# Kernel tuning notes

Hardware: AMD Instinct MI355X
Metric: run time of the kernel (lower is better)

Reference implementation:

```python
import jax, jax.numpy as jnp
import numpy as np

B, P, D, A = 256, 196, 512, 512

def setup_inputs() -> dict:
    key = jax.random.key(0)
    ks = jax.random.split(key, 12)
    sc = 1.0 / np.sqrt(D)
    sa = 1.0 / np.sqrt(A)
    return {
        "encoder_out": jax.random.normal(ks[0], (B, P, D), jnp.float32),
        "decoder_hidden": jax.random.normal(ks[1], (B, D), jnp.float32),
        "st": jax.random.normal(ks[2], (B, D), jnp.float32),
        "Wv": jax.random.normal(ks[3], (D, A), jnp.float32) * sc,
        "bv": jnp.zeros((A,), jnp.float32),
        "Wh": jax.random.normal(ks[4], (D, A), jnp.float32) * sc,
        "bh": jnp.zeros((A,), jnp.float32),
        "Ws": jax.random.normal(ks[5], (D, A), jnp.float32) * sc,
        "bs": jnp.zeros((A,), jnp.float32),
        "Wav": jax.random.normal(ks[6], (A,), jnp.float32) * sa,
        "bav": jnp.zeros((), jnp.float32),
        "Was": jax.random.normal(ks[7], (A,), jnp.float32) * sa,
        "bas": jnp.zeros((), jnp.float32),
    }

def reference(encoder_out, decoder_hidden, st, Wv, bv, Wh, bh, Ws, bs, Wav, bav, Was, bas):
    # hidden: (B, A)
    hidden = decoder_hidden @ Wh + bh
    # v: (B, P, A)
    v = jnp.einsum('bpd,da->bpa', encoder_out, Wv) + bv
    # z_t: (B, P) -- additive attention scores over pixels
    z_t = jnp.einsum('bpa,a->bp', jnp.tanh(v + hidden[:, None, :]), Wav) + bav
    alpha_t = jax.nn.softmax(z_t, axis=1)
    # c_t: (B, D) -- attention-weighted encoding
    c_t = jnp.einsum('bpd,bp->bd', encoder_out, alpha_t)
    # sentinel branch: s (B, A), s_att (B, 1)
    s = st @ Ws + bs
    s_att = jnp.tanh(s + hidden) @ Was + bas  # (B,)
    z_t_extended = jnp.concatenate([z_t, s_att[:, None]], axis=1)  # (B, P+1)
    alpha_t_hat = jax.nn.softmax(z_t_extended, axis=1)
    beta_t = alpha_t_hat[:, -1:]  # (B, 1)
    c_hat_t = beta_t * st + (1.0 - beta_t) * c_t
    return (c_hat_t, alpha_t, beta_t)
```

## Files before the change

kernel.cpp:

```cpp
#include <hip/hip_runtime.h>
#include <hip/hip_bf16.h>
#include <cstdint>

#define B_ 256
#define P_ 196
#define D_ 512
#define A_ 512

#define OUT_CHAT  0
#define OUT_ALPHA (B_*D_)
#define OUT_BETA  (B_*D_ + B_*P_)

typedef unsigned short ushort_t;
typedef uint32_t u32;
typedef uint64_t u64;
typedef __attribute__((ext_vector_type(8))) __bf16 bf16x8;
typedef __attribute__((ext_vector_type(4))) float f32x4;

__device__ __forceinline__ ushort_t f2bf(float f) {
    union { float f; u32 i; } v; v.f = f;
    u32 r = (v.i + 0x7fffu + ((v.i >> 16) & 1u)) >> 16;
    return (ushort_t)r;
}
__device__ __forceinline__ float bfbits2f(u32 lo16) {
    union { u32 i; float f; } v; v.i = lo16 << 16; return v.f;
}
__device__ __forceinline__ u32 cvt2bf(float x, float y) {
    union { __hip_bfloat162 h; u32 u; } v;
    v.h = __float22bfloat162_rn(make_float2(x, y));
    return v.u;
}
__device__ __forceinline__ float tanh_fast(float x) {
    float e = __expf(2.0f * x);
    return 1.0f - 2.0f / (e + 1.0f);
}
__device__ __forceinline__ void async_load16(const ushort_t* g, ushort_t* l) {
    __builtin_amdgcn_global_load_lds(
        (const __attribute__((address_space(1))) unsigned int*)g,
        (__attribute__((address_space(3))) unsigned int*)l, 16, 0, 0);
}
__device__ __forceinline__ void fma8(float ap, uint4 v, float ac[8]) {
    ac[0] = fmaf(ap, bfbits2f(v.x & 0xffffu), ac[0]);
    ac[1] = fmaf(ap, bfbits2f(v.x >> 16),     ac[1]);
    ac[2] = fmaf(ap, bfbits2f(v.y & 0xffffu), ac[2]);
    ac[3] = fmaf(ap, bfbits2f(v.y >> 16),     ac[3]);
    ac[4] = fmaf(ap, bfbits2f(v.z & 0xffffu), ac[4]);
    ac[5] = fmaf(ap, bfbits2f(v.z >> 16),     ac[5]);
    ac[6] = fmaf(ap, bfbits2f(v.w & 0xffffu), ac[6]);
    ac[7] = fmaf(ap, bfbits2f(v.w >> 16),     ac[7]);
}

__global__ __launch_bounds__(256) void k_prep(
    const float* __restrict__ E, const float* __restrict__ dh,
    const float* __restrict__ st,
    const float* __restrict__ Wv, const float* __restrict__ Wh,
    const float* __restrict__ Ws,
    ushort_t* __restrict__ Ebf, ushort_t* __restrict__ dhbf,
    ushort_t* __restrict__ stbf,
    ushort_t* __restrict__ WvT, ushort_t* __restrict__ WhT,
    ushort_t* __restrict__ WsT)
{
    __shared__ ushort_t tile[32][33];
    int bx = blockIdx.x;
    if (bx < 12544) {
        size_t i0 = (size_t)bx * 512 + threadIdx.x;
        const float4* src = (const float4*)E;
        u64* dst = (u64*)Ebf;
        float4 v0 = src[i0];
        float4 v1 = src[i0 + 256];
        dst[i0]       = (u64)cvt2bf(v0.x, v0.y) | ((u64)cvt2bf(v0.z, v0.w) << 32);
        dst[i0 + 256] = (u64)cvt2bf(v1.x, v1.y) | ((u64)cvt2bf(v1.z, v1.w) << 32);
    } else if (bx < 12672) {
        int gid = (bx - 12544) * 256 + threadIdx.x;
        float4 dv = ((const float4*)dh)[gid];
        float4 sv = ((const float4*)st)[gid];
        ((u64*)dhbf)[gid] = (u64)cvt2bf(dv.x, dv.y) | ((u64)cvt2bf(dv.z, dv.w) << 32);
        ((u64*)stbf)[gid] = (u64)cvt2bf(sv.x, sv.y) | ((u64)cvt2bf(sv.z, sv.w) << 32);
    } else {
        int idx = bx - 12672;
        int z   = idx >> 8;
        int rem = idx & 255;
        int tby = rem >> 4, tbx = rem & 15;
        const float* W  = (z == 0) ? Wv  : (z == 1) ? Wh  : Ws;
        ushort_t*    WT = (z == 0) ? WvT : (z == 1) ? WhT : WsT;
        int t = threadIdx.x, r = t >> 5, c = t & 31;
#pragma unroll
        for (int i = 0; i < 4; ++i) {
            int row = r + 8 * i;
            tile[row][c] = f2bf(W[(size_t)(tby * 32 + row) * A_ + tbx * 32 + c]);
        }
        __syncthreads();
#pragma unroll
        for (int i = 0; i < 4; ++i) {
            int row = r + 8 * i;
            WT[(size_t)(tbx * 32 + row) * D_ + tby * 32 + c] = tile[c][row];
        }
    }
}

#define PADK 72

__global__ __launch_bounds__(256) void k1_mfma(
    const ushort_t* __restrict__ dhbf, const ushort_t* __restrict__ stbf,
    const ushort_t* __restrict__ WhT,  const ushort_t* __restrict__ WsT,
    const float* __restrict__ bh, const float* __restrict__ bs,
    float* __restrict__ hidden_ws, float* __restrict__ s_ws)
{
    __shared__ ushort_t As[128 * PADK];
    __shared__ ushort_t Bs[128 * PADK];

    int mat = blockIdx.z;
    const ushort_t* Abf = mat ? stbf : dhbf;
    const ushort_t* WT  = mat ? WsT  : WhT;
    const float*    bia = mat ? bs   : bh;
    float*          outp = mat ? s_ws : hidden_ws;

    int tid = threadIdx.x;
    int m0 = blockIdx.y * 128;
    int n0 = blockIdx.x * 128;

    int lane = tid & 63, w = tid >> 6;
    int wm = w & 1, wn = w >> 1;
    int col = lane & 15, q = lane >> 4;

    f32x4 acc[4][4];
#pragma unroll
    for (int tm = 0; tm < 4; ++tm)
#pragma unroll
        for (int tn = 0; tn < 4; ++tn)
            acc[tm][tn] = (f32x4){0.f, 0.f, 0.f, 0.f};

    const ushort_t* arow = As + (wm * 64 + col) * PADK + q * 8;
    const ushort_t* brow = Bs + (wn * 64 + col) * PADK + q * 8;

    int sr = tid >> 3, sc = tid & 7;
    for (int kt = 0; kt < D_ / 64; ++kt) {
#pragma unroll
        for (int i = 0; i < 4; ++i) {
            int row = sr + i * 32;
            *(uint4*)(As + row * PADK + sc * 8) =
                *(const uint4*)(Abf + (size_t)(m0 + row) * D_ + kt * 64 + sc * 8);
            *(uint4*)(Bs + row * PADK + sc * 8) =
                *(const uint4*)(WT + (size_t)(n0 + row) * D_ + kt * 64 + sc * 8);
        }
        __syncthreads();
#pragma unroll
        for (int ks = 0; ks < 2; ++ks) {
            bf16x8 afr[4];
#pragma unroll
            for (int tm = 0; tm < 4; ++tm)
                afr[tm] = *(const bf16x8*)(arow + tm * 16 * PADK + ks * 32);
#pragma unroll
            for (int tn = 0; tn < 4; ++tn) {
                bf16x8 bfr = *(const bf16x8*)(brow + tn * 16 * PADK + ks * 32);
#pragma unroll
                for (int tm = 0; tm < 4; ++tm)
                    acc[tm][tn] = __builtin_amdgcn_mfma_f32_16x16x32_bf16(
                        afr[tm], bfr, acc[tm][tn], 0, 0, 0);
            }
        }
        __syncthreads();
    }

#pragma unroll
    for (int tm = 0; tm < 4; ++tm)
#pragma unroll
        for (int r = 0; r < 4; ++r) {
            int b = m0 + wm * 64 + tm * 16 + q * 4 + r;
#pragma unroll
            for (int tn = 0; tn < 4; ++tn) {
                int n = n0 + wn * 64 + tn * 16 + col;
                outp[(size_t)b * A_ + n] = acc[tm][tn][r] + bia[n];
            }
        }
}

#define BM3 64
__global__ __launch_bounds__(256, 2) void k2_z_bf(
    const ushort_t* __restrict__ Ebf, const ushort_t* __restrict__ WvT,
    const float* __restrict__ hidden_ws, const float* __restrict__ bv,
    const float* __restrict__ Wav, float* __restrict__ z_ws)
{
    __shared__ ushort_t As[BM3 * 512];
    __shared__ float hv_s[2][A_];
    __shared__ float wav_s[A_];
    __shared__ float zpart[4][BM3];

    int tid = threadIdx.x;
    int m0 = blockIdx.x * BM3;
    int b0 = m0 / P_, b1 = (m0 + BM3 - 1) / P_;

#pragma unroll
    for (int j = 0; j < 2; ++j) {
        int a = j * 256 + tid;
        float bva = bv[a];
        hv_s[0][a] = hidden_ws[(size_t)b0 * A_ + a] + bva;
        hv_s[1][a] = hidden_ws[(size_t)b1 * A_ + a] + bva;
        wav_s[a]   = Wav[a];
    }

    int lane = tid & 63, w = tid >> 6;
    int col = lane & 15, q = lane >> 4;

    {
        int r0 = tid >> 6, sc = tid & 63;
#pragma unroll
        for (int i = 0; i < 16; ++i) {
            int row  = i * 4 + r0;
            int slot = sc ^ (row & 7);
            async_load16(Ebf + (size_t)(m0 + row) * D_ + slot * 8,
                         As + i * 2048 + tid * 8);
        }
    }
    asm volatile("s_waitcnt vmcnt(0)" ::: "memory");
    __builtin_amdgcn_s_barrier();

    f32x4 acc[4][8];
#pragma unroll
    for (int tm = 0; tm < 4; ++tm)
#pragma unroll
        for (int tn = 0; tn < 8; ++tn)
            acc[tm][tn] = (f32x4){0.f, 0.f, 0.f, 0.f};

    int fx = col & 7;
    const ushort_t* bgp = WvT + (size_t)(w * 128 + col) * D_ + q * 8;

#pragma unroll
    for (int k32 = 0; k32 < 16; ++k32) {
        bf16x8 afr[4];
#pragma unroll
        for (int tm = 0; tm < 4; ++tm)
            afr[tm] = *(const bf16x8*)(As + (tm * 16 + col) * 512
                                          + (((k32 * 4 + q) ^ fx) * 8));
#pragma unroll
        for (int tn = 0; tn < 8; ++tn) {
            bf16x8 bfr = *(const bf16x8*)(bgp + (size_t)tn * 16 * D_ + k32 * 32);
#pragma unroll
            for (int tm = 0; tm < 4; ++tm)
                acc[tm][tn] = __builtin_amdgcn_mfma_f32_16x16x32_bf16(
                    afr[tm], bfr, acc[tm][tn], 0, 0, 0);
        }
    }

#pragma unroll
    for (int tm = 0; tm < 4; ++tm) {
#pragma unroll
        for (int r = 0; r < 4; ++r) {
            int row = tm * 16 + q * 4 + r;
            int bsel = ((m0 + row) / P_) - b0;
            float zr = 0.f;
#pragma unroll
            for (int tn = 0; tn < 8; ++tn) {
                int nl = w * 128 + tn * 16 + col;
                zr += wav_s[nl] * tanh_fast(acc[tm][tn][r] + hv_s[bsel][nl]);
            }
#pragma unroll
            for (int msk = 1; msk < 16; msk <<= 1)
                zr += __shfl_xor(zr, msk, 64);
            if (col == 0) zpart[w][row] = zr;
        }
    }
    __syncthreads();
    if (tid < BM3)
        z_ws[m0 + tid] = zpart[0][tid] + zpart[1][tid]
                       + zpart[2][tid] + zpart[3][tid];
}

__global__ __launch_bounds__(512) void k34_softmax_ct(
    const ushort_t* __restrict__ Ebf, const float* __restrict__ st,
    const float* __restrict__ z_ws, const float* __restrict__ hidden_ws,
    const float* __restrict__ s_ws, const float* __restrict__ Was,
    const float* __restrict__ bas, const float* __restrict__ bav,
    float* __restrict__ out)
{
    __shared__ float red[8];
    __shared__ float al[P_];
    __shared__ float acc_s[8][516];
    __shared__ float bm_s, bl_s, sa_s;

    int b = blockIdx.x, t = threadIdx.x;
    int lane = t & 63, w = t >> 6;

    float part = Was[t] * tanh_fast(s_ws[(size_t)b * A_ + t]
                                  + hidden_ws[(size_t)b * A_ + t]);
#pragma unroll
    for (int o = 32; o >= 1; o >>= 1) part += __shfl_down(part, o, 64);
    if (lane == 0) red[w] = part;
    __syncthreads();
    if (t == 0) {
        float s = 0.f;
#pragma unroll
        for (int i = 0; i < 8; ++i) s += red[i];
        sa_s = s + bas[0];
    }
    __syncthreads();

    float zv = (t < P_) ? (z_ws[(size_t)b * P_ + t] + bav[0]) : -1e30f;
    float m = zv;
#pragma unroll
    for (int o = 32; o >= 1; o >>= 1) m = fmaxf(m, __shfl_xor(m, o, 64));
    if (lane == 0) red[w] = m;
    __syncthreads();
    if (t == 0) {
        float mm = red[0];
#pragma unroll
        for (int i = 1; i < 8; ++i) mm = fmaxf(mm, red[i]);
        bm_s = mm;
    }
    __syncthreads();
    float m1 = bm_s;
    float e = (t < P_) ? __expf(zv - m1) : 0.f;
    float s = e;
#pragma unroll
    for (int o = 32; o >= 1; o >>= 1) s += __shfl_xor(s, o, 64);
    if (lane == 0) red[w] = s;
    __syncthreads();
    if (t == 0) {
        float ss = 0.f;
#pragma unroll
        for (int i = 0; i < 8; ++i) ss += red[i];
        bl_s = ss;
    }
    __syncthreads();
    float l1 = bl_s;
    if (t < P_) {
        float alpha = e / l1;
        al[t] = alpha;
        out[OUT_ALPHA + (size_t)b * P_ + t] = alpha;
    }
    float sa = sa_s;
    float m2 = fmaxf(m1, sa);
    float eb2 = __expf(sa - m2);
    float l2 = __expf(m1 - m2) * l1 + eb2;
    float beta = eb2 / l2;
    if (t == 0) out[OUT_BETA + b] = beta;
    __syncthreads();

    float ac[8] = {0.f, 0.f, 0.f, 0.f, 0.f, 0.f, 0.f, 0.f};
    const uint4* eb = (const uint4*)(Ebf + (size_t)b * P_ * D_);
#pragma unroll 4
    for (int i = 0; i < 24; ++i) {
        int pp = w + 8 * i;
        uint4 v = eb[(size_t)pp * (D_ / 8) + lane];
        fma8(al[pp], v, ac);
    }
    if (w < P_ - 192) {
        int pp = 192 + w;
        uint4 v = eb[(size_t)pp * (D_ / 8) + lane];
        fma8(al[pp], v, ac);
    }
#pragma unroll
    for (int j = 0; j < 8; ++j) acc_s[w][lane * 8 + j] = ac[j];
    __syncthreads();
    float c = 0.f;
#pragma unroll
    for (int g = 0; g < 8; ++g) c += acc_s[g][t];
    float sv = st[(size_t)b * D_ + t];
    out[OUT_CHAT + (size_t)b * D_ + t] = beta * sv + (1.f - beta) * c;
}

extern "C" void kernel_launch(void* const* d_in, const int* in_sizes, int n_in,
                              void* d_out, int out_size, void* d_ws, size_t ws_size,
                              hipStream_t stream)
{
    (void)in_sizes; (void)n_in; (void)out_size; (void)ws_size;
    const float* E   = (const float*)d_in[0];
    const float* dh  = (const float*)d_in[1];
    const float* st  = (const float*)d_in[2];
    const float* Wv  = (const float*)d_in[3];
    const float* bv  = (const float*)d_in[4];
    const float* Wh  = (const float*)d_in[5];
    const float* bh  = (const float*)d_in[6];
    const float* Ws  = (const float*)d_in[7];
    const float* bs  = (const float*)d_in[8];
    const float* Wav = (const float*)d_in[9];
    const float* bav = (const float*)d_in[10];
    const float* Was = (const float*)d_in[11];
    const float* bas = (const float*)d_in[12];
    float* out = (float*)d_out;

    char* ws = (char*)d_ws;
    ushort_t* WvT     = (ushort_t*)(ws);
    ushort_t* WhT     = (ushort_t*)(ws + 524288);
    ushort_t* WsT     = (ushort_t*)(ws + 1048576);
    float*    z_w     = (float*)(ws + 524288);
    ushort_t* dhbf    = (ushort_t*)(ws + 1572864);
    ushort_t* stbf    = (ushort_t*)(ws + 1835008);
    float*    hidden_w= (float*)(ws + 2097152);
    float*    s_w     = (float*)(ws + 2621440);
    ushort_t* Ebf     = (ushort_t*)(ws + 3145728);

    k_prep<<<12544 + 128 + 768, 256, 0, stream>>>(E, dh, st, Wv, Wh, Ws,
                                                  Ebf, dhbf, stbf, WvT, WhT, WsT);
    k1_mfma<<<dim3(4, 2, 2), 256, 0, stream>>>(dhbf, stbf, WhT, WsT, bh, bs,
                                               hidden_w, s_w);
    k2_z_bf<<<(B_ * P_) / BM3, 256, 0, stream>>>(
        Ebf, WvT, hidden_w, bv, Wav, z_w);
    k34_softmax_ct<<<256, 512, 0, stream>>>(Ebf, st, z_w, hidden_w, s_w,
                                            Was, bas, bav, out);
}
```

Baseline: 289.3 us.

## Split k2 score GEMM across 8 waves with 2x4 warp tiling

Doubles the k2_z_bf block to 512 threads and splits the 64-row tile across two wave rows, so each wave computes 32 rows by 128 columns instead of 64 by 128. The LDS A tile is reorganised into eight K-slices of 64 columns each, with an XOR swizzle, to match the new per-thread load pattern. This halves per-wave accumulator registers and adds waves to hide latency, but each WvT B fragment is now loaded by two waves, doubling global B traffic per block.

```diff
diff --git a/kernel.cpp b/kernel.cpp
--- a/kernel.cpp
+++ b/kernel.cpp
@@ -176,12 +176,12 @@
 }
 
 #define BM3 64
-__global__ __launch_bounds__(256, 2) void k2_z_bf(
+__global__ __launch_bounds__(512) void k2_z_bf(
     const ushort_t* __restrict__ Ebf, const ushort_t* __restrict__ WvT,
     const float* __restrict__ hidden_ws, const float* __restrict__ bv,
     const float* __restrict__ Wav, float* __restrict__ z_ws)
 {
-    __shared__ ushort_t As[BM3 * 512];
+    __shared__ ushort_t As[8][BM3 * 64];
     __shared__ float hv_s[2][A_];
     __shared__ float wav_s[A_];
     __shared__ float zpart[4][BM3];
@@ -190,9 +190,8 @@
     int m0 = blockIdx.x * BM3;
     int b0 = m0 / P_, b1 = (m0 + BM3 - 1) / P_;
 
-#pragma unroll
-    for (int j = 0; j < 2; ++j) {
-        int a = j * 256 + tid;
+    {
+        int a = tid;
         float bva = bv[a];
         hv_s[0][a] = hidden_ws[(size_t)b0 * A_ + a] + bva;
         hv_s[1][a] = hidden_ws[(size_t)b1 * A_ + a] + bva;
@@ -200,64 +199,64 @@
     }
 
     int lane = tid & 63, w = tid >> 6;
+    int wm = w & 1, wn = w >> 1;
     int col = lane & 15, q = lane >> 4;
 
     {
-        int r0 = tid >> 6, sc = tid & 63;
-#pragma unroll
-        for (int i = 0; i < 16; ++i) {
-            int row  = i * 4 + r0;
-            int slot = sc ^ (row & 7);
-            async_load16(Ebf + (size_t)(m0 + row) * D_ + slot * 8,
-                         As + i * 2048 + tid * 8);
-        }
+        int sr = tid >> 3, spos = tid & 7;
+        int gch = spos ^ (sr & 7);
+        const ushort_t* agb = Ebf + (size_t)(m0 + sr) * D_ + gch * 8;
+#pragma unroll
+        for (int kt = 0; kt < 8; ++kt)
+            async_load16(agb + kt * 64, &As[kt][0] + tid * 8);
     }
     asm volatile("s_waitcnt vmcnt(0)" ::: "memory");
     __builtin_amdgcn_s_barrier();
 
-    f32x4 acc[4][8];
-#pragma unroll
-    for (int tm = 0; tm < 4; ++tm)
+    f32x4 acc[2][8];
+#pragma unroll
+    for (int tm = 0; tm < 2; ++tm)
 #pragma unroll
         for (int tn = 0; tn < 8; ++tn)
             acc[tm][tn] = (f32x4){0.f, 0.f, 0.f, 0.f};
 
     int fx = col & 7;
-    const ushort_t* bgp = WvT + (size_t)(w * 128 + col) * D_ + q * 8;
+    const ushort_t* bgp = WvT + (size_t)(wn * 128 + col) * D_ + q * 8;
 
 #pragma unroll
     for (int k32 = 0; k32 < 16; ++k32) {
-        bf16x8 afr[4];
-#pragma unroll
-        for (int tm = 0; tm < 4; ++tm)
-            afr[tm] = *(const bf16x8*)(As + (tm * 16 + col) * 512
-                                          + (((k32 * 4 + q) ^ fx) * 8));
+        int kt = k32 >> 1, ks = k32 & 1;
+        bf16x8 afr[2];
+#pragma unroll
+        for (int tm = 0; tm < 2; ++tm)
+            afr[tm] = *(const bf16x8*)(&As[kt][0]
+                + (wm * 32 + tm * 16 + col) * 64 + (((ks * 4 + q) ^ fx) * 8));
 #pragma unroll
         for (int tn = 0; tn < 8; ++tn) {
             bf16x8 bfr = *(const bf16x8*)(bgp + (size_t)tn * 16 * D_ + k32 * 32);
 #pragma unroll
-            for (int tm = 0; tm < 4; ++tm)
+            for (int tm = 0; tm < 2; ++tm)
                 acc[tm][tn] = __builtin_amdgcn_mfma_f32_16x16x32_bf16(
                     afr[tm], bfr, acc[tm][tn], 0, 0, 0);
         }
     }
 
 #pragma unroll
-    for (int tm = 0; tm < 4; ++tm) {
+    for (int tm = 0; tm < 2; ++tm) {
 #pragma unroll
         for (int r = 0; r < 4; ++r) {
-            int row = tm * 16 + q * 4 + r;
+            int row = wm * 32 + tm * 16 + q * 4 + r;
             int bsel = ((m0 + row) / P_) - b0;
             float zr = 0.f;
 #pragma unroll
             for (int tn = 0; tn < 8; ++tn) {
-                int nl = w * 128 + tn * 16 + col;
+                int nl = wn * 128 + tn * 16 + col;
                 zr += wav_s[nl] * tanh_fast(acc[tm][tn][r] + hv_s[bsel][nl]);
             }
 #pragma unroll
             for (int msk = 1; msk < 16; msk <<= 1)
                 zr += __shfl_xor(zr, msk, 64);
-            if (col == 0) zpart[w][row] = zr;
+            if (col == 0) zpart[wn][row] = zr;
         }
     }
     __syncthreads();
@@ -394,7 +393,7 @@
                                                   Ebf, dhbf, stbf, WvT, WhT, WsT);
     k1_mfma<<<dim3(4, 2, 2), 256, 0, stream>>>(dhbf, stbf, WhT, WsT, bh, bs,
                                                hidden_w, s_w);
-    k2_z_bf<<<(B_ * P_) / BM3, 256, 0, stream>>>(
+    k2_z_bf<<<(B_ * P_) / BM3, 512, 0, stream>>>(
         Ebf, WvT, hidden_w, bv, Wav, z_w);
     k34_softmax_ct<<<256, 512, 0, stream>>>(Ebf, st, z_w, hidden_w, s_w,
                                             Was, bas, bav, out);
```

Result: slower. 331.9 us (+14.7%).
